# Kernel optimization log

Hardware: AMD Instinct MI355X
Metric: run time of the kernel (lower is better)

Reference implementation:

```python
import jax, jax.numpy as jnp
import numpy as np

E, B, S, P, D, H, HD, L, FF, NC = 4, 16, 224, 16, 384, 6, 64, 12, 1536, 10
NP = (S // P) ** 2  # 196 patches
T = NP + 1          # +cls token = 197


def _ln(x, w, b):
    m = x.mean(-1, keepdims=True)
    v = ((x - m) ** 2).mean(-1, keepdims=True)
    return (x - m) * jax.lax.rsqrt(v + 1e-6) * w + b


def setup_inputs() -> dict:
    key = jax.random.key(0)
    ks = iter(jax.random.split(key, 64))
    def rn(shape, s=0.02):
        return jax.random.normal(next(ks), shape, jnp.float32) * s
    return dict(
        x=jax.random.normal(next(ks), (B, 3, S, S), jnp.float32),
        gate_w=rn((3 * S * S, E)), gate_b=jnp.zeros((E,), jnp.float32),
        patch_w=rn((E, 3 * P * P, D)), patch_b=jnp.zeros((E, D), jnp.float32),
        cls=rn((E, 1, D)), pos=rn((E, T, D)),
        ln1_w=jnp.ones((E, L, D), jnp.float32), ln1_b=jnp.zeros((E, L, D), jnp.float32),
        qkv_w=rn((E, L, D, 3 * D)), qkv_b=jnp.zeros((E, L, 3 * D), jnp.float32),
        proj_w=rn((E, L, D, D)), proj_b=jnp.zeros((E, L, D), jnp.float32),
        ln2_w=jnp.ones((E, L, D), jnp.float32), ln2_b=jnp.zeros((E, L, D), jnp.float32),
        fc1_w=rn((E, L, D, FF)), fc1_b=jnp.zeros((E, L, FF), jnp.float32),
        fc2_w=rn((E, L, FF, D)), fc2_b=jnp.zeros((E, L, D), jnp.float32),
        norm_w=jnp.ones((E, D), jnp.float32), norm_b=jnp.zeros((E, D), jnp.float32),
        head_w=rn((E, D, NC)), head_b=jnp.zeros((E, NC), jnp.float32),
    )


def _vit(p, x):
    # one ViT-small expert (params p without expert axis) applied to batch x [b,3,S,S]
    b = x.shape[0]
    # patch embed: conv stride=kernel=16 == per-patch linear on [3*16*16]
    xp = x.reshape(b, 3, S // P, P, S // P, P).transpose(0, 2, 4, 1, 3, 5).reshape(b, NP, 3 * P * P)
    t = xp @ p['patch_w'] + p['patch_b']                                      # [b,196,384]
    t = jnp.concatenate([jnp.broadcast_to(p['cls'], (b, 1, D)), t], axis=1) + p['pos']  # [b,197,384]
    scale = 1.0 / np.sqrt(HD).astype(np.float32)

    def block(t, bp):
        h = _ln(t, bp['ln1_w'], bp['ln1_b'])
        qkv = (h @ bp['qkv_w'] + bp['qkv_b']).reshape(b, T, 3, H, HD)
        q, k, v = qkv[:, :, 0], qkv[:, :, 1], qkv[:, :, 2]
        a = jax.nn.softmax(jnp.einsum('bqhd,bkhd->bhqk', q, k) * scale, axis=-1)
        o = jnp.einsum('bhqk,bkhd->bqhd', a, v).reshape(b, T, D)
        t = t + o @ bp['proj_w'] + bp['proj_b']
        h2 = _ln(t, bp['ln2_w'], bp['ln2_b'])
        t = t + jax.nn.gelu(h2 @ bp['fc1_w'] + bp['fc1_b'], approximate=False) @ bp['fc2_w'] + bp['fc2_b']
        return t, None

    blk_keys = ('ln1_w', 'ln1_b', 'qkv_w', 'qkv_b', 'proj_w', 'proj_b',
                'ln2_w', 'ln2_b', 'fc1_w', 'fc1_b', 'fc2_w', 'fc2_b')
    blocks = {k: p[k] for k in blk_keys}  # each [L, ...] -> scanned over depth
    t, _ = jax.lax.scan(jax.checkpoint(block), t, blocks)
    t = _ln(t, p['norm_w'], p['norm_b'])
    return t[:, 0] @ p['head_w'] + p['head_b']  # cls-token head -> [b,10]


def reference(x, gate_w, gate_b, patch_w, patch_b, cls, pos,
              ln1_w, ln1_b, qkv_w, qkv_b, proj_w, proj_b,
              ln2_w, ln2_b, fc1_w, fc1_b, fc2_w, fc2_b,
              norm_w, norm_b, head_w, head_b):
    b = x.shape[0]
    logits = x.reshape(b, -1) @ gate_w + gate_b      # [B,E]
    idx = jnp.argmax(logits, axis=1)                 # top-1 expert per sample
    ep = dict(patch_w=patch_w, patch_b=patch_b, cls=cls, pos=pos,
              ln1_w=ln1_w, ln1_b=ln1_b, qkv_w=qkv_w, qkv_b=qkv_b,
              proj_w=proj_w, proj_b=proj_b, ln2_w=ln2_w, ln2_b=ln2_b,
              fc1_w=fc1_w, fc1_b=fc1_b, fc2_w=fc2_w, fc2_b=fc2_b,
              norm_w=norm_w, norm_b=norm_b, head_w=head_w, head_b=head_b)
    outs = jax.vmap(_vit, in_axes=(0, None))(ep, x)  # [E,B,10]: every expert on full batch
    return outs[idx, jnp.arange(b)]                  # per-sample top-1 select -> [B,10]
```

## Files before the change

### kernel.cpp

```cpp
#include <hip/hip_runtime.h>
#include <math.h>

#define E_ 4
#define B_ 16
#define S_ 224
#define P_ 16
#define D_ 384
#define H_ 6
#define HD_ 64
#define L_ 12
#define FF_ 1536
#define NC_ 10
#define NP_ 196
#define T_ 197
#define GATE_K (3 * S_ * S_)
#define GSPLIT 32
#define GCHUNK (GATE_K / GSPLIT)

typedef __attribute__((ext_vector_type(8))) short bf16x8;
typedef __attribute__((ext_vector_type(4))) float f32x4;

__device__ inline unsigned short f2bf(float f) {
  union { float f; unsigned u; } v; v.f = f;
  unsigned r = v.u + 0x7FFFu + ((v.u >> 16) & 1u);
  return (unsigned short)(r >> 16);
}

__global__ __launch_bounds__(256) void gate_partial(const float* __restrict__ x,
                                                    const float* __restrict__ gw,
                                                    float4* __restrict__ part) {
  int b = blockIdx.x, s = blockIdx.y, tid = threadIdx.x;
  const float* xb = x + (size_t)b * GATE_K;
  const float4* gw4 = (const float4*)gw;
  int i0 = s * GCHUNK, i1 = i0 + GCHUNK;
  float4 acc = make_float4(0.f, 0.f, 0.f, 0.f);
  for (int i = i0 + tid; i < i1; i += 256) {
    float xv = xb[i];
    float4 w = gw4[i];
    acc.x += xv * w.x; acc.y += xv * w.y; acc.z += xv * w.z; acc.w += xv * w.w;
  }
  __shared__ float4 red[256];
  red[tid] = acc;
  __syncthreads();
  for (int off = 128; off > 0; off >>= 1) {
    if (tid < off) {
      float4 o = red[tid + off];
      red[tid].x += o.x; red[tid].y += o.y; red[tid].z += o.z; red[tid].w += o.w;
    }
    __syncthreads();
  }
  if (tid == 0) part[b * GSPLIT + s] = red[0];
}

__global__ void gate_reduce(const float4* __restrict__ part, const float* __restrict__ gb,
                            int* __restrict__ idx) {
  int b = blockIdx.x;
  int lane = threadIdx.x;
  float4 a = make_float4(0.f, 0.f, 0.f, 0.f);
  if (lane < GSPLIT) a = part[b * GSPLIT + lane];
#pragma unroll
  for (int off = 1; off < 64; off <<= 1) {
    a.x += __shfl_xor(a.x, off);
    a.y += __shfl_xor(a.y, off);
    a.z += __shfl_xor(a.z, off);
    a.w += __shfl_xor(a.w, off);
  }
  if (lane == 0) {
    float v[4] = {a.x + gb[0], a.y + gb[1], a.z + gb[2], a.w + gb[3]};
    int best = 0;
    for (int e = 1; e < 4; ++e) if (v[e] > v[best]) best = e;
    idx[b] = best;
  }
}

__global__ void cls_kernel(const float* __restrict__ cls, const float* __restrict__ pos,
                           const int* __restrict__ idx, float* __restrict__ t) {
  int b = blockIdx.x;
  int d = threadIdx.x;
  int e = idx[b];
  t[((size_t)b * T_) * D_ + d] = cls[e * D_ + d] + pos[((size_t)e * T_) * D_ + d];
}

__global__ __launch_bounds__(256) void im2col_kernel(const float* __restrict__ x,
                                                     unsigned short* __restrict__ xpb) {
  int m = blockIdx.x, b = blockIdx.y, tid = threadIdx.x;
  int pr = m / 14, pc = m - pr * 14;
#pragma unroll
  for (int i = 0; i < 3; ++i) {
    int j = tid + i * 256;
    int c = j >> 8, y = (j >> 4) & 15, xx = j & 15;
    float v = x[(((size_t)b * 3 + c) * S_ + pr * 16 + y) * S_ + pc * 16 + xx];
    xpb[((size_t)b * NP_ + m) * 768 + j] = f2bf(v);
  }
}

__device__ inline void trans_tile_64(const float* __restrict__ src, int srcN,
                                     unsigned short* __restrict__ dst, int dstK,
                                     int k0, int n0, int tid) {
  __shared__ unsigned short tile[64][64];
  int rr = tid >> 4, c4 = (tid & 15) * 4;
#pragma unroll
  for (int p = 0; p < 4; ++p) {
    int row = p * 16 + rr;
    float4 v = *(const float4*)(src + (size_t)(k0 + row) * srcN + n0 + c4);
    ushort4 o;
    o.x = f2bf(v.x); o.y = f2bf(v.y); o.z = f2bf(v.z); o.w = f2bf(v.w);
    *(ushort4*)&tile[row][c4 ^ (row & 56)] = o;
  }
  __syncthreads();
  int n = tid >> 3, k8 = (tid & 7) * 8;
#pragma unroll
  for (int p = 0; p < 2; ++p) {
    int nn = p * 32 + n;
    union { unsigned short us[8]; uint4 u4; } o;
#pragma unroll
    for (int j = 0; j < 8; ++j) {
      int row = k8 + j;
      o.us[j] = tile[row][nn ^ (row & 56)];
    }
    *(uint4*)(dst + (size_t)(n0 + nn) * dstK + k0 + k8) = o.u4;
  }
}

__global__ __launch_bounds__(256) void ptrans_kernel(const float* __restrict__ pw,
                                                     unsigned short* __restrict__ tpw) {
  int e = blockIdx.y;
  int r = blockIdx.x;
  const int K = 768, N = 384;
  int kt = r / 6, nt = r - kt * 6;
  trans_tile_64(pw + (size_t)e * K * N, N, tpw + (size_t)e * N * K, K,
                kt * 64, nt * 64, threadIdx.x);
}

__global__ __launch_bounds__(256) void wtrans_kernel(
    const float* __restrict__ qw, const float* __restrict__ pw,
    const float* __restrict__ f1, const float* __restrict__ f2,
    unsigned short* __restrict__ tq, unsigned short* __restrict__ tp,
    unsigned short* __restrict__ t1, unsigned short* __restrict__ t2, int lsrc_base) {
  int e = blockIdx.y;
  int slot = blockIdx.z;
  int l = lsrc_base + slot;
  int r = blockIdx.x;
  const float* src; unsigned short* dst; int K, N, kt, nt;
  if (r < 108) {
    K = 384; N = 1152;
    src = qw + (size_t)(e * L_ + l) * K * N; dst = tq + (size_t)(slot * E_ + e) * K * N;
    kt = r / 18; nt = r % 18;
  } else if (r < 144) {
    r -= 108; K = 384; N = 384;
    src = pw + (size_t)(e * L_ + l) * K * N; dst = tp + (size_t)(slot * E_ + e) * K * N;
    kt = r / 6; nt = r % 6;
  } else if (r < 288) {
    r -= 144; K = 384; N = 1536;
    src = f1 + (size_t)(e * L_ + l) * K * N; dst = t1 + (size_t)(slot * E_ + e) * K * N;
    kt = r / 24; nt = r % 24;
  } else {
    r -= 288; K = 1536; N = 384;
    src = f2 + (size_t)(e * L_ + l) * K * N; dst = t2 + (size_t)(slot * E_ + e) * K * N;
    kt = r / 6; nt = r % 6;
  }
  trans_tile_64(src, N, dst, K, kt * 64, nt * 64, threadIdx.x);
}

__global__ void ln_kernel(const float* __restrict__ in, unsigned short* __restrict__ out,
                          const float* __restrict__ w, const float* __restrict__ bc,
                          const int* __restrict__ idx, int l) {
  int b = blockIdx.y;
  int row = blockIdx.x * 4 + (threadIdx.x >> 6);
  if (row >= T_) return;
  int lane = threadIdx.x & 63;
  int e = idx[b];
  const float* rp = in + ((size_t)b * T_ + row) * D_;
  float v[6];
  float s = 0.f;
#pragma unroll
  for (int j = 0; j < 6; ++j) { v[j] = rp[lane + j * 64]; s += v[j]; }
#pragma unroll
  for (int off = 1; off < 64; off <<= 1) s += __shfl_xor(s, off);
  float mean = s * (1.f / 384.f);
  float sq = 0.f;
#pragma unroll
  for (int j = 0; j < 6; ++j) { float dd = v[j] - mean; sq += dd * dd; }
#pragma unroll
  for (int off = 1; off < 64; off <<= 1) sq += __shfl_xor(sq, off);
  float rs = rsqrtf(sq * (1.f / 384.f) + 1e-6f);
  const float* wrow = w + ((size_t)e * L_ + l) * D_;
  const float* brow = bc + ((size_t)e * L_ + l) * D_;
  unsigned short* op = out + ((size_t)b * T_ + row) * D_;
#pragma unroll
  for (int j = 0; j < 6; ++j) {
    int d = lane + j * 64;
    op[d] = f2bf((v[j] - mean) * rs * wrow[d] + brow[d]);
  }
}

template <int EPI>
__global__ __launch_bounds__(256, 4) void gemm_mfma(
    const unsigned short* __restrict__ A, const unsigned short* __restrict__ WT,
    const float* __restrict__ bias, void* __restrict__ Out,
    const int* __restrict__ idx, int l, int K, int N, int M, size_t asb,
    int bstride, const float* __restrict__ pos) {
  int b = blockIdx.z;
  int e = idx[b];
  int n0 = blockIdx.x * 64, m0 = blockIdx.y * 64;
  int tid = threadIdx.x;
  const unsigned short* Ab = A + (size_t)b * asb;
  const unsigned short* Wb = WT + (size_t)e * N * K;
  __shared__ unsigned short Asl[8][64][8];
  __shared__ unsigned short Bsl[8][64][8];
  f32x4 acc[2][2];
#pragma unroll
  for (int i = 0; i < 2; ++i)
#pragma unroll
    for (int j = 0; j < 2; ++j) acc[i][j] = (f32x4){0.f, 0.f, 0.f, 0.f};
  int wid = tid >> 6, lane = tid & 63;
  int wm = (wid >> 1) * 32, wn = (wid & 1) * 32;
  int lrow = lane & 15, lk = lane >> 4;
  int ar = tid >> 2, akq = tid & 3;
  for (int k0 = 0; k0 < K; k0 += 64) {
    uint4 av0 = make_uint4(0, 0, 0, 0), av1 = av0;
    if (m0 + ar < M) {
      const unsigned short* ap = Ab + (size_t)(m0 + ar) * K + k0 + akq * 8;
      av0 = *(const uint4*)(ap);
      av1 = *(const uint4*)(ap + 32);
    }
    const unsigned short* bp = Wb + (size_t)(n0 + ar) * K + k0 + akq * 8;
    uint4 bv0 = *(const uint4*)(bp);
    uint4 bv1 = *(const uint4*)(bp + 32);
    __syncthreads();
    *(uint4*)&Asl[akq][ar][0] = av0;
    *(uint4*)&Asl[akq + 4][ar][0] = av1;
    *(uint4*)&Bsl[akq][ar][0] = bv0;
    *(uint4*)&Bsl[akq + 4][ar][0] = bv1;
    __syncthreads();
#pragma unroll
    for (int ks = 0; ks < 2; ++ks) {
      bf16x8 a0 = *(const bf16x8*)&Asl[ks * 4 + lk][wm + lrow][0];
      bf16x8 a1 = *(const bf16x8*)&Asl[ks * 4 + lk][wm + 16 + lrow][0];
      bf16x8 b0 = *(const bf16x8*)&Bsl[ks * 4 + lk][wn + lrow][0];
      bf16x8 b1 = *(const bf16x8*)&Bsl[ks * 4 + lk][wn + 16 + lrow][0];
      acc[0][0] = __builtin_amdgcn_mfma_f32_16x16x32_bf16(a0, b0, acc[0][0], 0, 0, 0);
      acc[0][1] = __builtin_amdgcn_mfma_f32_16x16x32_bf16(a0, b1, acc[0][1], 0, 0, 0);
      acc[1][0] = __builtin_amdgcn_mfma_f32_16x16x32_bf16(a1, b0, acc[1][0], 0, 0, 0);
      acc[1][1] = __builtin_amdgcn_mfma_f32_16x16x32_bf16(a1, b1, acc[1][1], 0, 0, 0);
    }
  }
  const float* brow = bias + ((size_t)e * bstride + l) * N + n0;
#pragma unroll
  for (int fm = 0; fm < 2; ++fm)
#pragma unroll
    for (int fn = 0; fn < 2; ++fn) {
      int col = wn + fn * 16 + lrow;
      float bval = brow[col];
#pragma unroll
      for (int r = 0; r < 4; ++r) {
        int row = m0 + wm + fm * 16 + lk * 4 + r;
        if (row >= M) continue;
        float val = acc[fm][fn][r] + bval;
        if (EPI == 0) {
          ((float*)Out)[((size_t)b * T_ + row) * N + n0 + col] = val;
        } else if (EPI == 1) {
          float* p = (float*)Out + ((size_t)b * T_ + row) * N + n0 + col;
          *p = *p + val;
        } else if (EPI == 2) {
          val = 0.5f * val * (1.f + erff(val * 0.70710678118654752f));
          ((unsigned short*)Out)[((size_t)b * T_ + row) * N + n0 + col] = f2bf(val);
        } else if (EPI == 3) {
          ((unsigned short*)Out)[((size_t)b * T_ + row) * N + n0 + col] = f2bf(val);
        } else {
          ((float*)Out)[((size_t)b * T_ + 1 + row) * N + n0 + col] =
              val + pos[((size_t)e * T_ + 1 + row) * N + n0 + col];
        }
      }
    }
}

__global__ __launch_bounds__(128, 2) void attn_mfma(const unsigned short* __restrict__ qkvb,
                                                    unsigned short* __restrict__ ob) {
  int b = blockIdx.z, h = blockIdx.y, qt = blockIdx.x;
  int tid = threadIdx.x;
  int w = tid >> 6, lane = tid & 63;
  int q0 = qt * 32 + w * 16;
  __shared__ unsigned short Vt[64][232];
  __shared__ unsigned short Pl[2][16][232];
  const unsigned short* base = qkvb + (size_t)b * T_ * (3 * D_) + h * HD_;

  {
    int d2 = (tid & 31) * 2;
    int kvh = tid >> 5;
    const unsigned short* vb = base + 2 * D_;
    for (int i = 0; i < 56; ++i) {
      int kv = kvh * 56 + i;
      int kvc = kv < T_ ? kv : T_ - 1;
      unsigned int vv = *(const unsigned int*)(vb + (size_t)kvc * (3 * D_) + d2);
      Vt[d2][kv] = (unsigned short)(vv & 0xffffu);
      Vt[d2 + 1][kv] = (unsigned short)(vv >> 16);
    }
  }

  int c16 = lane & 15, g4 = lane >> 4;

  int qrow = q0 + c16; if (qrow > T_ - 1) qrow = T_ - 1;
  bf16x8 aq[2];
#pragma unroll
  for (int ks = 0; ks < 2; ++ks)
    aq[ks] = *(const bf16x8*)(base + (size_t)qrow * (3 * D_) + ks * 32 + g4 * 8);

  f32x4 sc[14];
#pragma unroll
  for (int nf = 0; nf < 14; ++nf) sc[nf] = (f32x4){0.f, 0.f, 0.f, 0.f};
  const unsigned short* kb = base + D_;
#pragma unroll
  for (int nf = 0; nf < 14; ++nf) {
    int krow = nf * 16 + c16; if (krow > T_ - 1) krow = T_ - 1;
#pragma unroll
    for (int ks = 0; ks < 2; ++ks) {
      bf16x8 bk = *(const bf16x8*)(kb + (size_t)krow * (3 * D_) + ks * 32 + g4 * 8);
      sc[nf] = __builtin_amdgcn_mfma_f32_16x16x32_bf16(aq[ks], bk, sc[nf], 0, 0, 0);
    }
  }

  float mx[4], sm[4];
#pragma unroll
  for (int r = 0; r < 4; ++r) mx[r] = -1e30f;
#pragma unroll
  for (int nf = 0; nf < 14; ++nf) {
    bool valid = (nf * 16 + c16) < T_;
#pragma unroll
    for (int r = 0; r < 4; ++r) {
      float s = valid ? sc[nf][r] * 0.125f : -1e30f;
      sc[nf][r] = s;
      mx[r] = fmaxf(mx[r], s);
    }
  }
#pragma unroll
  for (int r = 0; r < 4; ++r) {
#pragma unroll
    for (int off = 1; off < 16; off <<= 1) mx[r] = fmaxf(mx[r], __shfl_xor(mx[r], off, 16));
    sm[r] = 0.f;
  }
#pragma unroll
  for (int nf = 0; nf < 14; ++nf)
#pragma unroll
    for (int r = 0; r < 4; ++r) {
      float p = __expf(sc[nf][r] - mx[r]);
      sc[nf][r] = p;
      sm[r] += p;
    }
#pragma unroll
  for (int r = 0; r < 4; ++r) {
#pragma unroll
    for (int off = 1; off < 16; off <<= 1) sm[r] += __shfl_xor(sm[r], off, 16);
    sm[r] = 1.f / sm[r];
  }
#pragma unroll
  for (int nf = 0; nf < 14; ++nf) {
    int col = nf * 16 + c16;
#pragma unroll
    for (int r = 0; r < 4; ++r)
      Pl[w][g4 * 4 + r][col] = f2bf(sc[nf][r] * sm[r]);
  }
  __syncthreads();

  f32x4 oacc[4];
#pragma unroll
  for (int nf = 0; nf < 4; ++nf) oacc[nf] = (f32x4){0.f, 0.f, 0.f, 0.f};
#pragma unroll
  for (int ks = 0; ks < 7; ++ks) {
    bf16x8 ap = *(const bf16x8*)&Pl[w][c16][ks * 32 + g4 * 8];
#pragma unroll
    for (int nf = 0; nf < 4; ++nf) {
      bf16x8 bv = *(const bf16x8*)&Vt[nf * 16 + c16][ks * 32 + g4 * 8];
      oacc[nf] = __builtin_amdgcn_mfma_f32_16x16x32_bf16(ap, bv, oacc[nf], 0, 0, 0);
    }
  }

#pragma unroll
  for (int nf = 0; nf < 4; ++nf) {
    int d = nf * 16 + c16;
#pragma unroll
    for (int r = 0; r < 4; ++r) {
      int q = q0 + g4 * 4 + r;
      if (q < T_)
        ob[((size_t)b * T_ + q) * D_ + h * HD_ + d] = f2bf(oacc[nf][r]);
    }
  }
}

__global__ void head_kernel(const float* __restrict__ t, const float* __restrict__ nw,
                            const float* __restrict__ nb, const float* __restrict__ hw,
                            const float* __restrict__ hb, const int* __restrict__ idx,
                            float* __restrict__ out) {
  int b = blockIdx.x;
  int e = idx[b];
  int lane = threadIdx.x;
  const float* rp = t + (size_t)b * T_ * D_;
  float v[6];
  float s = 0.f;
#pragma unroll
  for (int j = 0; j < 6; ++j) { v[j] = rp[lane + j * 64]; s += v[j]; }
#pragma unroll
  for (int off = 1; off < 64; off <<= 1) s += __shfl_xor(s, off);
  float mean = s * (1.f / 384.f);
  float sq = 0.f;
#pragma unroll
  for (int j = 0; j < 6; ++j) { float dd = v[j] - mean; sq += dd * dd; }
#pragma unroll
  for (int off = 1; off < 64; off <<= 1) sq += __shfl_xor(sq, off);
  float rs = rsqrtf(sq * (1.f / 384.f) + 1e-6f);
  __shared__ float ln[D_];
#pragma unroll
  for (int j = 0; j < 6; ++j) {
    int d = lane + j * 64;
    ln[d] = (v[j] - mean) * rs * nw[e * D_ + d] + nb[e * D_ + d];
  }
  __syncthreads();
  if (lane < NC_) {
    float acc = hb[e * NC_ + lane];
    for (int d = 0; d < D_; ++d) acc += ln[d] * hw[((size_t)e * D_ + d) * NC_ + lane];
    out[b * NC_ + lane] = acc;
  }
}

extern "C" void kernel_launch(void* const* d_in, const int* in_sizes, int n_in,
                              void* d_out, int out_size, void* d_ws, size_t ws_size,
                              hipStream_t stream) {
  const float* x      = (const float*)d_in[0];
  const float* gate_w = (const float*)d_in[1];
  const float* gate_b = (const float*)d_in[2];
  const float* patch_w = (const float*)d_in[3];
  const float* patch_b = (const float*)d_in[4];
  const float* cls    = (const float*)d_in[5];
  const float* pos    = (const float*)d_in[6];
  const float* ln1_w  = (const float*)d_in[7];
  const float* ln1_b  = (const float*)d_in[8];
  const float* qkv_w  = (const float*)d_in[9];
  const float* qkv_b  = (const float*)d_in[10];
  const float* proj_w = (const float*)d_in[11];
  const float* proj_b = (const float*)d_in[12];
  const float* ln2_w  = (const float*)d_in[13];
  const float* ln2_b  = (const float*)d_in[14];
  const float* fc1_w  = (const float*)d_in[15];
  const float* fc1_b  = (const float*)d_in[16];
  const float* fc2_w  = (const float*)d_in[17];
  const float* fc2_b  = (const float*)d_in[18];
  const float* norm_w = (const float*)d_in[19];
  const float* norm_b = (const float*)d_in[20];
  const float* head_w = (const float*)d_in[21];
  const float* head_b = (const float*)d_in[22];

  const size_t SQ = (size_t)D_ * 3 * D_, SP = (size_t)D_ * D_;
  const size_t S1 = (size_t)D_ * FF_, S2 = (size_t)FF_ * D_;
  const size_t WSET = SQ + SP + S1 + S2;

  float* ws = (float*)d_ws;
  int* idx = (int*)ws;
  float4* gpart = (float4*)(ws + 64);
  float* t = ws + 64 + 4 * B_ * GSPLIT;
  unsigned short* qkvb = (unsigned short*)(t + (size_t)B_ * T_ * D_);
  unsigned short* hbuf = qkvb + (size_t)B_ * T_ * 3 * D_;
  unsigned short* ob = hbuf + (size_t)B_ * T_ * D_;
  unsigned short* ub = ob + (size_t)B_ * T_ * D_;
  unsigned short* xpb = ub + (size_t)B_ * T_ * FF_;
  unsigned short* tpw = xpb + (size_t)B_ * NP_ * 768;
  unsigned short* wbase = tpw + (size_t)E_ * D_ * 768;
  size_t fixed_bytes = (size_t)((char*)wbase - (char*)d_ws);
  bool hoist = ws_size >= fixed_bytes + WSET * 2ull * E_ * L_ + 4096;
  int NL = hoist ? L_ : 1;
  unsigned short* tq = wbase;
  unsigned short* tp = tq + (size_t)NL * E_ * SQ;
  unsigned short* t1 = tp + (size_t)NL * E_ * SP;
  unsigned short* t2 = t1 + (size_t)NL * E_ * S1;

  gate_partial<<<dim3(B_, GSPLIT), 256, 0, stream>>>(x, gate_w, gpart);
  gate_reduce<<<B_, 64, 0, stream>>>(gpart, gate_b, idx);
  cls_kernel<<<B_, D_, 0, stream>>>(cls, pos, idx, t);
  im2col_kernel<<<dim3(NP_, B_), 256, 0, stream>>>(x, xpb);
  ptrans_kernel<<<dim3(72, E_), 256, 0, stream>>>(patch_w, tpw);
  if (hoist)
    wtrans_kernel<<<dim3(432, E_, L_), 256, 0, stream>>>(qkv_w, proj_w, fc1_w, fc2_w,
                                                         tq, tp, t1, t2, 0);
  gemm_mfma<4><<<dim3(6, 4, B_), 256, 0, stream>>>(
      xpb, tpw, patch_b, t, idx, 0, 768, D_, NP_, (size_t)NP_ * 768, 1, pos);

  for (int l = 0; l < L_; ++l) {
    int slot = hoist ? l : 0;
    if (!hoist)
      wtrans_kernel<<<dim3(432, E_, 1), 256, 0, stream>>>(qkv_w, proj_w, fc1_w, fc2_w,
                                                          tq, tp, t1, t2, l);
    unsigned short* tql = tq + (size_t)slot * E_ * SQ;
    unsigned short* tpl = tp + (size_t)slot * E_ * SP;
    unsigned short* t1l = t1 + (size_t)slot * E_ * S1;
    unsigned short* t2l = t2 + (size_t)slot * E_ * S2;
    ln_kernel<<<dim3(50, B_), 256, 0, stream>>>(t, hbuf, ln1_w, ln1_b, idx, l);
    gemm_mfma<3><<<dim3(18, 4, B_), 256, 0, stream>>>(
        hbuf, tql, qkv_b, qkvb, idx, l, D_, 3 * D_, T_, (size_t)T_ * D_, L_, nullptr);
    attn_mfma<<<dim3(7, H_, B_), 128, 0, stream>>>(qkvb, ob);
    gemm_mfma<1><<<dim3(6, 4, B_), 256, 0, stream>>>(
        ob, tpl, proj_b, t, idx, l, D_, D_, T_, (size_t)T_ * D_, L_, nullptr);
    ln_kernel<<<dim3(50, B_), 256, 0, stream>>>(t, hbuf, ln2_w, ln2_b, idx, l);
    gemm_mfma<2><<<dim3(24, 4, B_), 256, 0, stream>>>(
        hbuf, t1l, fc1_b, ub, idx, l, D_, FF_, T_, (size_t)T_ * D_, L_, nullptr);
    gemm_mfma<1><<<dim3(6, 4, B_), 256, 0, stream>>>(
        ub, t2l, fc2_b, t, idx, l, FF_, D_, T_, (size_t)T_ * FF_, L_, nullptr);
  }
  head_kernel<<<B_, 64, 0, stream>>>(t, norm_w, norm_b, head_w, head_b, idx, (float*)d_out);
}
```

Measured before the change: 1.269 ms.

## Prefetch next K-tile into registers and add BM=32 tile variant for narrow GEMMs

The GEMM kernel now loads the next K-slice of A and B into registers while the current slice is consumed by MFMAs, overlapping global loads with compute. A template parameter BM lets the N=384 GEMMs (patch, proj, fc2) use 32-row tiles, nearly doubling block count from 384 to 672 for better CU occupancy. The trade-off is more register pressure from the double set of staging registers, and more redundant B-tile loads for the smaller tiles.

```diff
diff --git a/kernel.cpp b/kernel.cpp
--- a/kernel.cpp
+++ b/kernel.cpp
@@ -194,60 +194,79 @@
   }
 }
 
-template <int EPI>
+template <int EPI, int BM>
 __global__ __launch_bounds__(256, 4) void gemm_mfma(
     const unsigned short* __restrict__ A, const unsigned short* __restrict__ WT,
     const float* __restrict__ bias, void* __restrict__ Out,
     const int* __restrict__ idx, int l, int K, int N, int M, size_t asb,
     int bstride, const float* __restrict__ pos) {
+  constexpr int MF = BM / 32;
   int b = blockIdx.z;
   int e = idx[b];
-  int n0 = blockIdx.x * 64, m0 = blockIdx.y * 64;
+  int n0 = blockIdx.x * 64, m0 = blockIdx.y * BM;
   int tid = threadIdx.x;
   const unsigned short* Ab = A + (size_t)b * asb;
   const unsigned short* Wb = WT + (size_t)e * N * K;
-  __shared__ unsigned short Asl[8][64][8];
+  __shared__ unsigned short Asl[8][BM][8];
   __shared__ unsigned short Bsl[8][64][8];
-  f32x4 acc[2][2];
-#pragma unroll
-  for (int i = 0; i < 2; ++i)
+  f32x4 acc[MF][2];
+#pragma unroll
+  for (int i = 0; i < MF; ++i)
 #pragma unroll
     for (int j = 0; j < 2; ++j) acc[i][j] = (f32x4){0.f, 0.f, 0.f, 0.f};
   int wid = tid >> 6, lane = tid & 63;
-  int wm = (wid >> 1) * 32, wn = (wid & 1) * 32;
+  int wm = (wid >> 1) * (BM / 2), wn = (wid & 1) * 32;
   int lrow = lane & 15, lk = lane >> 4;
-  int ar = tid >> 2, akq = tid & 3;
+  int arA, akqA;
+  if (BM == 64) { arA = tid >> 2; akqA = tid & 3; }
+  else          { arA = tid >> 3; akqA = tid & 7; }
+  int arB = tid >> 2, akqB = tid & 3;
+
+  uint4 a0c = make_uint4(0, 0, 0, 0), a1c = a0c, b0c, b1c;
+  uint4 a0n = a0c, a1n = a0c, b0n = a0c, b1n = a0c;
+  if (m0 + arA < M) {
+    const unsigned short* ap = Ab + (size_t)(m0 + arA) * K + akqA * 8;
+    a0c = *(const uint4*)ap;
+    if (BM == 64) a1c = *(const uint4*)(ap + 32);
+  }
+  {
+    const unsigned short* bp = Wb + (size_t)(n0 + arB) * K + akqB * 8;
+    b0c = *(const uint4*)bp;
+    b1c = *(const uint4*)(bp + 32);
+  }
   for (int k0 = 0; k0 < K; k0 += 64) {
-    uint4 av0 = make_uint4(0, 0, 0, 0), av1 = av0;
-    if (m0 + ar < M) {
-      const unsigned short* ap = Ab + (size_t)(m0 + ar) * K + k0 + akq * 8;
-      av0 = *(const uint4*)(ap);
-      av1 = *(const uint4*)(ap + 32);
-    }
-    const unsigned short* bp = Wb + (size_t)(n0 + ar) * K + k0 + akq * 8;
-    uint4 bv0 = *(const uint4*)(bp);
-    uint4 bv1 = *(const uint4*)(bp + 32);
     __syncthreads();
-    *(uint4*)&Asl[akq][ar][0] = av0;
-    *(uint4*)&Asl[akq + 4][ar][0] = av1;
-    *(uint4*)&Bsl[akq][ar][0] = bv0;
-    *(uint4*)&Bsl[akq + 4][ar][0] = bv1;
+    *(uint4*)&Asl[akqA][arA][0] = a0c;
+    if (BM == 64) *(uint4*)&Asl[akqA + 4][arA][0] = a1c;
+    *(uint4*)&Bsl[akqB][arB][0] = b0c;
+    *(uint4*)&Bsl[akqB + 4][arB][0] = b1c;
     __syncthreads();
+    if (k0 + 64 < K) {
+      if (m0 + arA < M) {
+        const unsigned short* ap = Ab + (size_t)(m0 + arA) * K + k0 + 64 + akqA * 8;
+        a0n = *(const uint4*)ap;
+        if (BM == 64) a1n = *(const uint4*)(ap + 32);
+      }
+      const unsigned short* bp = Wb + (size_t)(n0 + arB) * K + k0 + 64 + akqB * 8;
+      b0n = *(const uint4*)bp;
+      b1n = *(const uint4*)(bp + 32);
+    }
 #pragma unroll
     for (int ks = 0; ks < 2; ++ks) {
-      bf16x8 a0 = *(const bf16x8*)&Asl[ks * 4 + lk][wm + lrow][0];
-      bf16x8 a1 = *(const bf16x8*)&Asl[ks * 4 + lk][wm + 16 + lrow][0];
-      bf16x8 b0 = *(const bf16x8*)&Bsl[ks * 4 + lk][wn + lrow][0];
-      bf16x8 b1 = *(const bf16x8*)&Bsl[ks * 4 + lk][wn + 16 + lrow][0];
-      acc[0][0] = __builtin_amdgcn_mfma_f32_16x16x32_bf16(a0, b0, acc[0][0], 0, 0, 0);
-      acc[0][1] = __builtin_amdgcn_mfma_f32_16x16x32_bf16(a0, b1, acc[0][1], 0, 0, 0);
-      acc[1][0] = __builtin_amdgcn_mfma_f32_16x16x32_bf16(a1, b0, acc[1][0], 0, 0, 0);
-      acc[1][1] = __builtin_amdgcn_mfma_f32_16x16x32_bf16(a1, b1, acc[1][1], 0, 0, 0);
-    }
+      bf16x8 bb0 = *(const bf16x8*)&Bsl[ks * 4 + lk][wn + lrow][0];
+      bf16x8 bb1 = *(const bf16x8*)&Bsl[ks * 4 + lk][wn + 16 + lrow][0];
+#pragma unroll
+      for (int fm = 0; fm < MF; ++fm) {
+        bf16x8 aa = *(const bf16x8*)&Asl[ks * 4 + lk][wm + fm * 16 + lrow][0];
+        acc[fm][0] = __builtin_amdgcn_mfma_f32_16x16x32_bf16(aa, bb0, acc[fm][0], 0, 0, 0);
+        acc[fm][1] = __builtin_amdgcn_mfma_f32_16x16x32_bf16(aa, bb1, acc[fm][1], 0, 0, 0);
+      }
+    }
+    a0c = a0n; a1c = a1n; b0c = b0n; b1c = b1n;
   }
   const float* brow = bias + ((size_t)e * bstride + l) * N + n0;
 #pragma unroll
-  for (int fm = 0; fm < 2; ++fm)
+  for (int fm = 0; fm < MF; ++fm)
 #pragma unroll
     for (int fn = 0; fn < 2; ++fn) {
       int col = wn + fn * 16 + lrow;
@@ -480,7 +499,7 @@
   if (hoist)
     wtrans_kernel<<<dim3(432, E_, L_), 256, 0, stream>>>(qkv_w, proj_w, fc1_w, fc2_w,
                                                          tq, tp, t1, t2, 0);
-  gemm_mfma<4><<<dim3(6, 4, B_), 256, 0, stream>>>(
+  gemm_mfma<4, 32><<<dim3(6, 7, B_), 256, 0, stream>>>(
       xpb, tpw, patch_b, t, idx, 0, 768, D_, NP_, (size_t)NP_ * 768, 1, pos);
 
   for (int l = 0; l < L_; ++l) {
@@ -493,15 +512,15 @@
     unsigned short* t1l = t1 + (size_t)slot * E_ * S1;
     unsigned short* t2l = t2 + (size_t)slot * E_ * S2;
     ln_kernel<<<dim3(50, B_), 256, 0, stream>>>(t, hbuf, ln1_w, ln1_b, idx, l);
-    gemm_mfma<3><<<dim3(18, 4, B_), 256, 0, stream>>>(
+    gemm_mfma<3, 64><<<dim3(18, 4, B_), 256, 0, stream>>>(
         hbuf, tql, qkv_b, qkvb, idx, l, D_, 3 * D_, T_, (size_t)T_ * D_, L_, nullptr);
     attn_mfma<<<dim3(7, H_, B_), 128, 0, stream>>>(qkvb, ob);
-    gemm_mfma<1><<<dim3(6, 4, B_), 256, 0, stream>>>(
+    gemm_mfma<1, 32><<<dim3(6, 7, B_), 256, 0, stream>>>(
         ob, tpl, proj_b, t, idx, l, D_, D_, T_, (size_t)T_ * D_, L_, nullptr);
     ln_kernel<<<dim3(50, B_), 256, 0, stream>>>(t, hbuf, ln2_w, ln2_b, idx, l);
-    gemm_mfma<2><<<dim3(24, 4, B_), 256, 0, stream>>>(
+    gemm_mfma<2, 64><<<dim3(24, 4, B_), 256, 0, stream>>>(
         hbuf, t1l, fc1_b, ub, idx, l, D_, FF_, T_, (size_t)T_ * D_, L_, nullptr);
-    gemm_mfma<1><<<dim3(6, 4, B_), 256, 0, stream>>>(
+    gemm_mfma<1, 32><<<dim3(6, 7, B_), 256, 0, stream>>>(
         ub, t2l, fc2_b, t, idx, l, FF_, D_, T_, (size_t)T_ * FF_, L_, nullptr);
   }
   head_kernel<<<B_, 64, 0, stream>>>(t, norm_w, norm_b, head_w, head_b, idx, (float*)d_out);
```

Result: no change. 1.279 ms (+0.8%).
